# Kernel optimization log

Measured on AMD Instinct MI355X. Metric: run time of the kernel, lower is better.

Reference implementation:

```python
import jax, jax.numpy as jnp
import numpy as np

N = 50000   # nodes
E = 800000  # edges
F = 128     # feat_dim
I = 128     # internal_dim
G = 64      # graphs in batch
EPS = 1e-5


def setup_inputs() -> dict:
    key = jax.random.key(0)
    ks = jax.random.split(key, 32)
    s = 0.1
    inp = {
        'x': jax.random.normal(ks[0], (N, F), dtype=jnp.float32),
        'edge_index': jax.random.randint(ks[1], (2, E), 0, N, dtype=jnp.int64),
        'batch': jnp.sort(jax.random.randint(ks[2], (N,), 0, G, dtype=jnp.int64)),
        # InitialSubnet: Linear(F->I) + BN(I)
        'init_W': jax.random.normal(ks[3], (F, I)) * s,
        'init_b': jnp.zeros((I,)),
        'init_g': jnp.ones((I,)),
        'init_bt': jnp.zeros((I,)),
        # 2 middle EdgeConv subnets: Linear(2I->I) + BN(I)
        'mid_W': jax.random.normal(ks[4], (2, 2 * I, I)) * s,
        'mid_b': jnp.zeros((2, I)),
        'mid_g': jnp.ones((2, I)),
        'mid_bt': jnp.zeros((2, I)),
        # 1 er / 1 pr receptor-specific EdgeConv subnet each
        'er_W': jax.random.normal(ks[5], (1, 2 * I, I)) * s,
        'er_b': jnp.zeros((1, I)),
        'er_g': jnp.ones((1, I)),
        'er_bt': jnp.zeros((1, I)),
        'pr_W': jax.random.normal(ks[6], (1, 2 * I, I)) * s,
        'pr_b': jnp.zeros((1, I)),
        'pr_g': jnp.ones((1, I)),
        'pr_bt': jnp.zeros((1, I)),
        # 3 shared posts: Linear(I->2) + BN(2)
        'spost_W': jax.random.normal(ks[7], (3, I, 2)) * s,
        'spost_b': jnp.zeros((3, 2)),
        'spost_g': jnp.ones((3, 2)),
        'spost_bt': jnp.zeros((3, 2)),
        # 1 er post / 1 pr post: Linear(I->1) + BN(1)
        'erpost_W': jax.random.normal(ks[8], (1, I, 1)) * s,
        'erpost_b': jnp.zeros((1, 1)),
        'erpost_g': jnp.ones((1, 1)),
        'erpost_bt': jnp.zeros((1, 1)),
        'prpost_W': jax.random.normal(ks[9], (1, I, 1)) * s,
        'prpost_b': jnp.zeros((1, 1)),
        'prpost_g': jnp.ones((1, 1)),
        'prpost_bt': jnp.zeros((1, 1)),
    }
    return inp


def _bn(h, g, b):
    # BatchNorm1d in training mode: batch stats over the row dim, biased var
    m = jnp.mean(h, axis=0)
    v = jnp.var(h, axis=0)
    return (h - m) * jax.lax.rsqrt(v + EPS) * g + b


def _edgeconv(h, src, dst, W, b, g, bt):
    # PyG EdgeConv: msg = nn(cat([x_i, x_j - x_i])), aggr=max over incoming edges
    x_i = h[dst]                      # [E, I]
    x_j = h[src]                      # [E, I]
    msg = jnp.concatenate([x_i, x_j - x_i], axis=-1) @ W + b  # [E, I]
    msg = jax.nn.elu(_bn(msg, g, bt))
    out = jax.ops.segment_max(msg, dst, num_segments=N)
    return jnp.where(jnp.isneginf(out), 0.0, out)  # isolated nodes -> 0


def _post(h, batch, counts, W, b, g, bt):
    # elu(BN(Linear(h))) then global_mean_pool; dropout is identity (eval)
    h2 = jax.nn.elu(_bn(h @ W + b, g, bt))
    pooled = jax.ops.segment_sum(h2, batch, num_segments=G)
    return pooled / counts[:, None]


def reference(x, edge_index, batch,
              init_W, init_b, init_g, init_bt,
              mid_W, mid_b, mid_g, mid_bt,
              er_W, er_b, er_g, er_bt,
              pr_W, pr_b, pr_g, pr_bt,
              spost_W, spost_b, spost_g, spost_bt,
              erpost_W, erpost_b, erpost_g, erpost_bt,
              prpost_W, prpost_b, prpost_g, prpost_bt):
    src, dst = edge_index[0], edge_index[1]
    counts = jnp.maximum(jax.ops.segment_sum(jnp.ones((N,), x.dtype), batch, num_segments=G), 1.0)

    outs = []
    # InitialSubnet: gelu(BN(Linear(x)))
    h = jax.nn.gelu(_bn(x @ init_W + init_b, init_g, init_bt), approximate=False)
    outs.append(_post(h, batch, counts, spost_W[0], spost_b[0], spost_g[0], spost_bt[0]))

    for l in range(2):
        h = _edgeconv(h, src, dst, mid_W[l], mid_b[l], mid_g[l], mid_bt[l])
        outs.append(_post(h, batch, counts, spost_W[l + 1], spost_b[l + 1], spost_g[l + 1], spost_bt[l + 1]))

    er_h = h
    pr_h = h
    for l in range(1):
        er_h = _edgeconv(er_h, src, dst, er_W[l], er_b[l], er_g[l], er_bt[l])
        er_out = _post(er_h, batch, counts, erpost_W[l], erpost_b[l], erpost_g[l], erpost_bt[l])
        pr_h = _edgeconv(pr_h, src, dst, pr_W[l], pr_b[l], pr_g[l], pr_bt[l])
        pr_out = _post(pr_h, batch, counts, prpost_W[l], prpost_b[l], prpost_g[l], prpost_bt[l])
        outs.append(jnp.concatenate([er_out, pr_out], axis=-1))

    agg = outs[0]
    for o in outs[1:]:
        agg = agg + o
    return agg  # [G, 2]
```

## Files before the change

### kernel.cpp

```cpp
#include <hip/hip_runtime.h>
#include <math.h>

#define EPS 1e-5f

typedef float f32x4v __attribute__((ext_vector_type(4)));
typedef short s16x8  __attribute__((ext_vector_type(8)));

__device__ __forceinline__ float elu_f(float x) { return x > 0.f ? x : expm1f(x); }
__device__ __forceinline__ float blo(unsigned u) { return __uint_as_float(u << 16); }
__device__ __forceinline__ float bhi(unsigned u) { return __uint_as_float(u & 0xffff0000u); }
__device__ __forceinline__ unsigned f2b(float f) {
  unsigned u = __float_as_uint(f);
  unsigned r = ((u >> 16) & 1u) + 0x7fffu;
  return (u + r) >> 16;
}
__device__ __forceinline__ unsigned pack2(float a, float b) {
  return f2b(a) | (f2b(b) << 16);
}

__global__ __launch_bounds__(256) void prep_csr0(const float* __restrict__ init_W,
    const float* __restrict__ mid_W, const float* __restrict__ er_W,
    const float* __restrict__ pr_W, const float* __restrict__ mid_g,
    const float* __restrict__ er_g, const float* __restrict__ pr_g,
    unsigned short* __restrict__ WT,
// ... 12 lines not shown
    if (grp == 1)      { W = mid_W;             g = mid_g;       Wd = WT + 1 * 16384; W2 = WT + 2 * 16384; }
    else if (grp == 2) { W = mid_W + 256 * 128; g = mid_g + 128; Wd = WT + 3 * 16384; W2 = WT + 4 * 16384; }
    else if (grp == 3) { W = er_W;              g = er_g;        Wd = WT + 5 * 16384; W2 = WT + 6 * 16384; }
    else               { W = pr_W;              g = pr_g;        Wd = WT + 7 * 16384; W2 = WT + 8 * 16384; }
    float sg = (g[c] >= 0.f) ? 1.f : -1.f;
    float w1 = W[k * 128 + c];
    float w2 = W[(k + 128) * 128 + c];
    Wd[c * 128 + k] = (unsigned short)f2b((w1 - w2) * sg);
    W2[c * 128 + k] = (unsigned short)f2b(w2 * sg);
  } else {
    int b = blockIdx.x - 320;
    if (b < 64) {
      __shared__ int cnt[256];
      cnt[threadIdx.x] = 0;
      __syncthreads();
      int i0 = b * 256 + threadIdx.x, stride = 64 * 256;
      for (int e = i0; e < Ecnt; e += stride) atomicAdd(&cnt[(unsigned)dst[e] >> 8], 1);
      __syncthreads();
      partials[b * 256 + threadIdx.x] = cnt[threadIdx.x];
    } else {
      __shared__ float lc[64];
      if (threadIdx.x < 64) lc[threadIdx.x] = 0.f;
      __syncthreads();
      int i0 = (b - 64) * 256 + threadIdx.x, stride = 64 * 256;
      for (int n = i0; n < Nn; n += stride) atomicAdd(&lc[batch[n]], 1.f);
      __syncthreads();
      if (threadIdx.x < 64 && lc[threadIdx.x] != 0.f)
        atomicAdd(&counts[threadIdx.x * 16], lc[threadIdx.x]);
    }
  }
}

__global__ __launch_bounds__(256) void csr_p0_scan(const int* __restrict__ partials,
    int nblk, int* __restrict__ bucket_base, int* __restrict__ gcursor) {
  __shared__ int sc[256];
  int b = threadIdx.x;
  int s = 0;
  for (int k = 0; k < nblk; ++k) s += partials[k * 256 + b];
  sc[b] = s;
  __syncthreads();
  for (int off = 1; off < 256; off <<= 1) {
    int t = (b >= off) ? sc[b - off] : 0;
    __syncthreads();
    sc[b] += t;
    __syncthreads();
  }
  int excl = sc[b] - s;
  bucket_base[b] = excl;
  gcursor[b * 16] = excl;
  if (b == 255) bucket_base[256] = sc[255];
}

#define P1_CHUNK 4096
__global__ __launch_bounds__(256) void csr_p1_bin(const int* __restrict__ src,
    const int* __restrict__ dst, int* __restrict__ gcursor,
    unsigned* __restrict__ binned, int Ecnt) {
  __shared__ unsigned stage[P1_CHUNK];
  __shared__ int cnt[256], lbase[256], gbase[256], lcur[256], sc[256];
  int tid = threadIdx.x;
  int e0 = blockIdx.x * P1_CHUNK;
  int ecnt = Ecnt - e0; if (ecnt > P1_CHUNK) ecnt = P1_CHUNK;
  cnt[tid] = 0;
  __syncthreads();
  for (int i = tid; i < ecnt; i += 256) atomicAdd(&cnt[(unsigned)dst[e0 + i] >> 8], 1);
  __syncthreads();
  sc[tid] = cnt[tid];
  __syncthreads();
  for (int off = 1; off < 256; off <<= 1) {
    int t = (tid >= off) ? sc[tid - off] : 0;
    __syncthreads();
    sc[tid] += t;
    __syncthreads();
  }
  lbase[tid] = sc[tid] - cnt[tid];
  lcur[tid] = lbase[tid];
  gbase[tid] = (cnt[tid] > 0) ? atomicAdd(&gcursor[tid * 16], cnt[tid]) : 0;
  __syncthreads();
  for (int i = tid; i < ecnt; i += 256) {
    int d = dst[e0 + i], s = src[e0 + i];
    int bk = (unsigned)d >> 8;
    int p = atomicAdd(&lcur[bk], 1);
    stage[p] = ((unsigned)bk << 24) | ((unsigned)(d & 255) << 16) | (unsigned)s;
  }
  __syncthreads();
  for (int i = tid; i < ecnt; i += 256) {
    unsigned v = stage[i];
    int bk = v >> 24;
    binned[gbase[bk] + (i - lbase[bk])] = v;
  }
}

#define P2_CAP 12288
__global__ __launch_bounds__(256) void csr_p2_sort(const unsigned* __restrict__ binned,
    const int* __restrict__ bucket_base, unsigned short* __restrict__ csr_src,
    int* __restrict__ deg, int* __restrict__ rowstart, int Nn) {
  __shared__ unsigned short stage[P2_CAP];
  __shared__ int cnt[256], lbase[256], lcur[256], sc[256];
  int b = blockIdx.x, tid = threadIdx.x;
  int base = bucket_base[b];
  int bcnt = bucket_base[b + 1] - base;
  if (bcnt > P2_CAP) bcnt = P2_CAP;
  cnt[tid] = 0;
  __syncthreads();
  for (int i = tid; i < bcnt; i += 256) atomicAdd(&cnt[(binned[base + i] >> 16) & 255], 1);
  __syncthreads();
  sc[tid] = cnt[tid];
  __syncthreads();
  for (int off = 1; off < 256; off <<= 1) {
    int t = (tid >= off) ? sc[tid - off] : 0;
    __syncthreads();
    sc[tid] += t;
    __syncthreads();
  }
  lbase[tid] = sc[tid] - cnt[tid];
  lcur[tid] = lbase[tid];
  int node = b * 256 + tid;
  if (node < Nn) { deg[node] = cnt[tid]; rowstart[node] = base + lbase[tid]; }
  __syncthreads();
  for (int i = tid; i < bcnt; i += 256) {
    unsigned v = binned[base + i];
    int j = (v >> 16) & 255;
    int p = atomicAdd(&lcur[j], 1);
    stage[p] = (unsigned short)(v & 0xffffu);
  }
  __syncthreads();
  for (int i = tid; i < bcnt; i += 256) csr_src[base + i] = stage[i];
}

template<int XF32, int NMAT, int STATS>
__global__ __launch_bounds__(256, 3) void gemm_mfma(const void* __restrict__ Xv,
    const unsigned short* __restrict__ W0t, const unsigned short* __restrict__ W1t,
    const unsigned short* __restrict__ W2t, const unsigned short* __restrict__ W3t,
    unsigned short* __restrict__ Y0, unsigned short* __restrict__ Y1,
    unsigned short* __restrict__ Y2, unsigned short* __restrict__ Y3,
    float* __restrict__ stOut, int Nrows) {
  int tid = threadIdx.x, lane = tid & 63, wv = tid >> 6;
  int r0 = blockIdx.x * 64;
  int rlo = lane & 15, kg = lane >> 4;
  s16x8 zf = {0, 0, 0, 0, 0, 0, 0, 0};
  s16x8 af[4][4];
#pragma unroll
  for (int rg = 0; rg < 4; ++rg) {
    int arow = r0 + rg * 16 + rlo;
    if (arow < Nrows) {
      if (XF32) {
        const float* xr = (const float*)Xv + (size_t)arow * 128 + kg * 8;
#pragma unroll
        for (int s2 = 0; s2 < 4; ++s2) {
          float4 a = *(const float4*)(xr + s2 * 32);
          float4 b = *(const float4*)(xr + s2 * 32 + 4);
          s16x8 t;
          t[0] = (short)f2b(a.x); t[1] = (short)f2b(a.y);
          t[2] = (short)f2b(a.z); t[3] = (short)f2b(a.w);
          t[4] = (short)f2b(b.x); t[5] = (short)f2b(b.y);
          t[6] = (short)f2b(b.z); t[7] = (short)f2b(b.w);
          af[rg][s2] = t;
        }
      } else {
        const unsigned short* xr = (const unsigned short*)Xv + (size_t)arow * 128 + kg * 8;
#pragma unroll
        for (int s2 = 0; s2 < 4; ++s2) af[rg][s2] = *(const s16x8*)(xr + s2 * 32);
      }
    } else {
#pragma unroll
      for (int s2 = 0; s2 < 4; ++s2) af[rg][s2] = zf;
    }
  }
  const unsigned short* Ws[4] = {W0t, W1t, W2t, W3t};
  unsigned short* Ys[4] = {Y0, Y1, Y2, Y3};
#pragma unroll
  for (int o = 0; o < NMAT; ++o) {
    const unsigned short* Wt = Ws[o];
    unsigned short* Y = Ys[o];
#pragma unroll
    for (int t = 0; t < 2; ++t) {
      int nt = wv * 2 + t;
      const unsigned short* wp = Wt + (size_t)(nt * 16 + rlo) * 128 + kg * 8;
      s16x8 wf[4];
#pragma unroll
      for (int s2 = 0; s2 < 4; ++s2) wf[s2] = *(const s16x8*)(wp + s2 * 32);
      f32x4v acc[4];
#pragma unroll
      for (int rg = 0; rg < 4; ++rg) acc[rg] = (f32x4v){0.f, 0.f, 0.f, 0.f};
#pragma unroll
      for (int s2 = 0; s2 < 4; ++s2)
#pragma unroll
        for (int rg = 0; rg < 4; ++rg)
          acc[rg] = __builtin_amdgcn_mfma_f32_16x16x32_bf16(wf[s2], af[rg][s2], acc[rg], 0, 0, 0);
      float ps0 = 0.f, ps1 = 0.f, ps2 = 0.f, ps3 = 0.f;
      float pq0 = 0.f, pq1 = 0.f, pq2 = 0.f, pq3 = 0.f;
#pragma unroll
      for (int rg = 0; rg < 4; ++rg) {
        int arow = r0 + rg * 16 + rlo;
        if (arow < Nrows) {
          uint2 ov;
          ov.x = pack2(acc[rg][0], acc[rg][1]);
          ov.y = pack2(acc[rg][2], acc[rg][3]);
          *(uint2*)(Y + (size_t)arow * 128 + nt * 16 + kg * 4) = ov;
          if (STATS) {
            float y0 = blo(ov.x), y1 = bhi(ov.x), y2 = blo(ov.y), y3 = bhi(ov.y);
            ps0 += y0; pq0 += y0 * y0;
            ps1 += y1; pq1 += y1 * y1;
            ps2 += y2; pq2 += y2 * y2;
            ps3 += y3; pq3 += y3 * y3;
          }
        }
      }
      if (STATS) {
#pragma unroll
        for (int off = 1; off < 16; off <<= 1) {
          ps0 += __shfl_xor(ps0, off); pq0 += __shfl_xor(pq0, off);
          ps1 += __shfl_xor(ps1, off); pq1 += __shfl_xor(pq1, off);
          ps2 += __shfl_xor(ps2, off); pq2 += __shfl_xor(pq2, off);
          ps3 += __shfl_xor(ps3, off); pq3 += __shfl_xor(pq3, off);
        }
        if (rlo == 0) {
          int col = nt * 16 + kg * 4;
          float* sb = stOut + (size_t)(blockIdx.x & 15) * 256;
          atomicAdd(&sb[2 * col + 0], ps0); atomicAdd(&sb[2 * col + 1], pq0);
          atomicAdd(&sb[2 * (col + 1)], ps1); atomicAdd(&sb[2 * (col + 1) + 1], pq1);
          atomicAdd(&sb[2 * (col + 2)], ps2); atomicAdd(&sb[2 * (col + 2) + 1], pq2);
          atomicAdd(&sb[2 * (col + 3)], ps3); atomicAdd(&sb[2 * (col + 3) + 1], pq3);
        }
      }
    }
  }
}

template<int NMAT, int ACT>
__global__ __launch_bounds__(256, 3) void gemm_act(const unsigned short* __restrict__ Xv,
    const unsigned short* __restrict__ W0t, const unsigned short* __restrict__ W1t,
    const unsigned short* __restrict__ W2t, const unsigned short* __restrict__ W3t,
    unsigned short* __restrict__ Y0, unsigned short* __restrict__ Y1,
    unsigned short* __restrict__ Y2, unsigned short* __restrict__ Y3,
    const float* __restrict__ stn, const float* __restrict__ g,
    const float* __restrict__ bt, const int* __restrict__ deg,
    const float* __restrict__ Wp, float* __restrict__ zP, float* __restrict__ stp,
    float invCnt, int Nrows) {
  __shared__ unsigned short hl[64][136];
  __shared__ float lsc[128], lsh[128], lw0[128], lw1[128];
  __shared__ float red[4][4];
  int tid = threadIdx.x, lane = tid & 63, wv = tid >> 6;
  int r0 = blockIdx.x * 64;
  int rlo = lane & 15, kg = lane >> 4;
  if (tid < 128) {
    float sm = 0.f, sq = 0.f;
#pragma unroll
    for (int k = 0; k < 16; ++k) {
      sm += stn[k * 256 + 2 * tid];
      sq += stn[k * 256 + 2 * tid + 1];
    }
    float mean = sm * invCnt;
    float var = sq * invCnt - mean * mean;
    float sc = g[tid] * rsqrtf(var + EPS);
    float sh = bt[tid] - mean * sc;
    if (ACT == 2 && g[tid] < 0.f) sc = -sc;
    lsc[tid] = sc; lsh[tid] = sh;
    lw0[tid] = Wp[tid * 2]; lw1[tid] = Wp[tid * 2 + 1];
  }
  __syncthreads();
  {
    int row = tid >> 2, q = tid & 3;
    int arow = r0 + row;
    bool rok = arow < Nrows;
    int lrow = rok ? arow : 0;
    float live = 1.f;
    if (ACT == 2) live = (rok && deg[arow] > 0) ? 1.f : 0.f;
    else live = rok ? 1.f : 0.f;
    const uint4* xr = (const uint4*)(Xv + (size_t)lrow * 128 + q * 32);
    float dd0 = 0.f, dd1 = 0.f;
#pragma unroll
    for (int b = 0; b < 4; ++b) {
      uint4 v = xr[b];
      unsigned w[4] = {v.x, v.y, v.z, v.w};
      int cb = q * 32 + b * 8;
#pragma unroll
      for (int u = 0; u < 4; ++u) {
        int c = cb + 2 * u;
        float t0 = blo(w[u]) * lsc[c] + lsh[c];
        float t1 = bhi(w[u]) * lsc[c + 1] + lsh[c + 1];
        float y0, y1;
        if (ACT == 1) {
          y0 = 0.5f * t0 * (1.f + erff(t0 * 0.70710678118f));
          y1 = 0.5f * t1 * (1.f + erff(t1 * 0.70710678118f));
        } else {
          y0 = elu_f(t0); y1 = elu_f(t1);
        }
        y0 *= live; y1 *= live;
        *(unsigned*)&hl[row][c] = pack2(y0, y1);
        dd0 += y0 * lw0[c] + y1 * lw0[c + 1];
        dd1 += y0 * lw1[c] + y1 * lw1[c + 1];
      }
    }
    dd0 += __shfl_xor(dd0, 1); dd0 += __shfl_xor(dd0, 2);
    dd1 += __shfl_xor(dd1, 1); dd1 += __shfl_xor(dd1, 2);
    if (q == 0 && rok) {
// ... 3 lines not shown
    float s0v = (q == 0 && rok) ? dd0 : 0.f;
    float s1v = (q == 0 && rok) ? dd1 : 0.f;
    float q0v = s0v * s0v, q1v = s1v * s1v;
#pragma unroll
    for (int off = 4; off < 64; off <<= 1) {
      s0v += __shfl_xor(s0v, off); s1v += __shfl_xor(s1v, off);
      q0v += __shfl_xor(q0v, off); q1v += __shfl_xor(q1v, off);
    }
    if (lane == 0) { red[wv][0] = s0v; red[wv][1] = s1v; red[wv][2] = q0v; red[wv][3] = q1v; }
  }
  __syncthreads();
  if (tid < 4) {
    float v = red[0][tid] + red[1][tid] + red[2][tid] + red[3][tid];
    atomicAdd(&stp[tid * 64], v);
  }
  s16x8 af[4][4];
#pragma unroll
  for (int rg = 0; rg < 4; ++rg)
#pragma unroll
    for (int s2 = 0; s2 < 4; ++s2)
      af[rg][s2] = *(const s16x8*)&hl[rg * 16 + rlo][kg * 8 + s2 * 32];
  const unsigned short* Ws[4] = {W0t, W1t, W2t, W3t};
  unsigned short* Ys[4] = {Y0, Y1, Y2, Y3};
#pragma unroll
  for (int o = 0; o < NMAT; ++o) {
    const unsigned short* Wt = Ws[o];
    unsigned short* Y = Ys[o];
#pragma unroll
    for (int t = 0; t < 2; ++t) {
      int nt = wv * 2 + t;
      const unsigned short* wp = Wt + (size_t)(nt * 16 + rlo) * 128 + kg * 8;
      s16x8 wf[4];
#pragma unroll
      for (int s2 = 0; s2 < 4; ++s2) wf[s2] = *(const s16x8*)(wp + s2 * 32);
      f32x4v acc[4];
#pragma unroll
      for (int rg = 0; rg < 4; ++rg) acc[rg] = (f32x4v){0.f, 0.f, 0.f, 0.f};
#pragma unroll
      for (int s2 = 0; s2 < 4; ++s2)
#pragma unroll
        for (int rg = 0; rg < 4; ++rg)
          acc[rg] = __builtin_amdgcn_mfma_f32_16x16x32_bf16(wf[s2], af[rg][s2], acc[rg], 0, 0, 0);
#pragma unroll
      for (int rg = 0; rg < 4; ++rg) {
        int arow = r0 + rg * 16 + rlo;
        if (arow < Nrows) {
          uint2 ov;
          ov.x = pack2(acc[rg][0], acc[rg][1]);
          ov.y = pack2(acc[rg][2], acc[rg][3]);
          *(uint2*)(Y + (size_t)arow * 128 + nt * 16 + kg * 4) = ov;
        }
      }
    }
  }
}

__global__ __launch_bounds__(256, 8) void conv_pass(const unsigned short* __restrict__ A,
    const unsigned short* __restrict__ B, const unsigned short* __restrict__ csr_src,
    const int* __restrict__ rowstart, const int* __restrict__ deg,
    const float* __restrict__ g, unsigned short* __restrict__ Mx,
    float* __restrict__ st, int Nn, int convBlks,
    const float* __restrict__ zPp, const int* __restrict__ batch,
    const float* __restrict__ counts, const float* __restrict__ stpp,
    const float* __restrict__ g2, const float* __restrict__ bt2,
    float* __restrict__ out, float invN) {
  __shared__ float s_sum[128], s_ssq[128];
  int tid = threadIdx.x;
  if ((int)blockIdx.x >= convBlks) {
    __shared__ float lacc[128];
    if (tid < 128) lacc[tid] = 0.f;
    __syncthreads();
    float m0 = stpp[0] * invN, v0 = stpp[128] * invN - m0 * m0;
    float scale0 = g2[0] * rsqrtf(v0 + EPS), shift0 = bt2[0] - m0 * scale0;
    float m1 = stpp[64] * invN, v1 = stpp[192] * invN - m1 * m1;
    float scale1 = g2[1] * rsqrtf(v1 + EPS), shift1 = bt2[1] - m1 * scale1;
    int i0 = (blockIdx.x - convBlks) * 256 + tid;
    int stride = 32 * 256;
    for (int n = i0; n < Nn; n += stride) {
      int gi = batch[n];
      atomicAdd(&lacc[gi * 2], elu_f(zPp[n * 2] * scale0 + shift0));
      atomicAdd(&lacc[gi * 2 + 1], elu_f(zPp[n * 2 + 1] * scale1 + shift1));
    }
    __syncthreads();
    if (tid < 128) {
      int gi = tid >> 1, p = tid & 1;
      float v = lacc[tid];
      if (v != 0.f) atomicAdd(&out[gi * 2 + p], v / fmaxf(counts[gi * 16], 1.f));
    }
    return;
  }
  if (tid < 128) { s_sum[tid] = 0.f; s_ssq[tid] = 0.f; }
  __syncthreads();
  int lane = tid & 63;
  int wave = __builtin_amdgcn_readfirstlane((blockIdx.x << 2) + (tid >> 6));
  int wstride = convBlks << 2;
  int c0 = lane * 2;
  float sg0 = (g[c0] >= 0.f) ? 1.f : -1.f;
  float sg1 = (g[c0 + 1] >= 0.f) ? 1.f : -1.f;
  const unsigned* A32 = (const unsigned*)A;
  const unsigned* B32 = (const unsigned*)B;
  unsigned* M32 = (unsigned*)Mx;
  float s0 = 0.f, ss0 = 0.f, s1 = 0.f, ss1 = 0.f;
  for (int n = wave; n < Nn; n += wstride) {
    int dg = deg[n];
    if (dg == 0) continue;
    int beg = rowstart[n];
    unsigned ua = A32[(size_t)n * 64 + lane];
    float a0 = blo(ua), a1 = bhi(ua);
    float mx0 = -INFINITY, mx1 = -INFINITY;
    int e = beg, eend = beg + dg;
    for (; e + 8 <= eend; e += 8) {
      int idx[8];
#pragma unroll
      for (int q = 0; q < 8; ++q) idx[q] = csr_src[e + q];
      unsigned uu[8];
#pragma unroll
      for (int q = 0; q < 8; ++q) uu[q] = B32[(size_t)idx[q] * 64 + lane];
#pragma unroll
      for (int q = 0; q < 8; ++q) {
        float m0 = a0 + blo(uu[q]), m1 = a1 + bhi(uu[q]);
        s0 += m0; ss0 += m0 * m0;
        s1 += m1; ss1 += m1 * m1;
        mx0 = fmaxf(mx0, m0);
        mx1 = fmaxf(mx1, m1);
      }
    }
    for (; e + 2 <= eend; e += 2) {
      int ia = csr_src[e], ib = csr_src[e + 1];
      unsigned u0 = B32[(size_t)ia * 64 + lane];
      unsigned u1 = B32[(size_t)ib * 64 + lane];
      float m00 = a0 + blo(u0), m01 = a1 + bhi(u0);
      float m10 = a0 + blo(u1), m11 = a1 + bhi(u1);
      s0 += m00 + m10; ss0 += m00 * m00 + m10 * m10;
      s1 += m01 + m11; ss1 += m01 * m01 + m11 * m11;
      mx0 = fmaxf(mx0, fmaxf(m00, m10));
      mx1 = fmaxf(mx1, fmaxf(m01, m11));
    }
    if (e < eend) {
      unsigned u0 = B32[(size_t)csr_src[e] * 64 + lane];
      float m00 = a0 + blo(u0), m01 = a1 + bhi(u0);
      s0 += m00; ss0 += m00 * m00;
      s1 += m01; ss1 += m01 * m01;
      mx0 = fmaxf(mx0, m00);
      mx1 = fmaxf(mx1, m01);
    }
    M32[(size_t)n * 64 + lane] = pack2(mx0, mx1);
  }
  atomicAdd(&s_sum[c0], s0 * sg0); atomicAdd(&s_ssq[c0], ss0);
  atomicAdd(&s_sum[c0 + 1], s1 * sg1); atomicAdd(&s_ssq[c0 + 1], ss1);
  __syncthreads();
  if (tid < 128) {
    float* sb = st + (size_t)(blockIdx.x & 15) * 256;
    atomicAdd(&sb[2 * tid], s_sum[tid]);
    atomicAdd(&sb[2 * tid + 1], s_ssq[tid]);
  }
}

__global__ __launch_bounds__(256, 8) void conv_pass_dual(
    const unsigned short* __restrict__ Aer, const unsigned short* __restrict__ Ber,
    const unsigned short* __restrict__ Apr, const unsigned short* __restrict__ Bpr,
    const unsigned short* __restrict__ csr_src,
    const int* __restrict__ rowstart, const int* __restrict__ deg,
    const float* __restrict__ g_er, const float* __restrict__ g_pr,
    unsigned short* __restrict__ Mer, unsigned short* __restrict__ Mpr,
    float* __restrict__ st_er, float* __restrict__ st_pr, int Nn, int convBlks,
    const float* __restrict__ zPp, const int* __restrict__ batch,
    const float* __restrict__ counts, const float* __restrict__ stpp,
    const float* __restrict__ g2, const float* __restrict__ bt2,
    float* __restrict__ out, float invN) {
  __shared__ float s_e[256], s_p[256];
  int tid = threadIdx.x;
  if ((int)blockIdx.x >= convBlks) {
    __shared__ float lacc[128];
    if (tid < 128) lacc[tid] = 0.f;
    __syncthreads();
    float m0 = stpp[0] * invN, v0 = stpp[128] * invN - m0 * m0;
    float scale0 = g2[0] * rsqrtf(v0 + EPS), shift0 = bt2[0] - m0 * scale0;
    float m1 = stpp[64] * invN, v1 = stpp[192] * invN - m1 * m1;
    float scale1 = g2[1] * rsqrtf(v1 + EPS), shift1 = bt2[1] - m1 * scale1;
    int i0 = (blockIdx.x - convBlks) * 256 + tid;
    int stride = 32 * 256;
    for (int n = i0; n < Nn; n += stride) {
      int gi = batch[n];
      atomicAdd(&lacc[gi * 2], elu_f(zPp[n * 2] * scale0 + shift0));
      atomicAdd(&lacc[gi * 2 + 1], elu_f(zPp[n * 2 + 1] * scale1 + shift1));
    }
    __syncthreads();
    if (tid < 128) {
      int gi = tid >> 1, p = tid & 1;
      float v = lacc[tid];
      if (v != 0.f) atomicAdd(&out[gi * 2 + p], v / fmaxf(counts[gi * 16], 1.f));
    }
    return;
  }
  s_e[tid] = 0.f; s_p[tid] = 0.f;
  __syncthreads();
  int lane = tid & 63;
  int wave = __builtin_amdgcn_readfirstlane((blockIdx.x << 2) + (tid >> 6));
  int wstride = convBlks << 2;
  int c0 = lane * 2;
  float sge0 = (g_er[c0] >= 0.f) ? 1.f : -1.f;
  float sge1 = (g_er[c0 + 1] >= 0.f) ? 1.f : -1.f;
  float sgp0 = (g_pr[c0] >= 0.f) ? 1.f : -1.f;
  float sgp1 = (g_pr[c0 + 1] >= 0.f) ? 1.f : -1.f;
  const unsigned* Ae32 = (const unsigned*)Aer;
  const unsigned* Be32 = (const unsigned*)Ber;
  const unsigned* Ap32 = (const unsigned*)Apr;
  const unsigned* Bp32 = (const unsigned*)Bpr;
  unsigned* Me32 = (unsigned*)Mer;
  unsigned* Mp32 = (unsigned*)Mpr;
  float se0 = 0.f, sse0 = 0.f, se1 = 0.f, sse1 = 0.f;
  float sp0 = 0.f, ssp0 = 0.f, sp1 = 0.f, ssp1 = 0.f;
  for (int n = wave; n < Nn; n += wstride) {
    int dg = deg[n];
    if (dg == 0) continue;
    int beg = rowstart[n];
    unsigned uae = Ae32[(size_t)n * 64 + lane];
    unsigned uap = Ap32[(size_t)n * 64 + lane];
    float ae0 = blo(uae), ae1 = bhi(uae);
    float ap0 = blo(uap), ap1 = bhi(uap);
    float mxe0 = -INFINITY, mxe1 = -INFINITY, mxp0 = -INFINITY, mxp1 = -INFINITY;
    int e = beg, eend = beg + dg;
    for (; e + 8 <= eend; e += 8) {
      int idx[8];
#pragma unroll
      for (int q = 0; q < 8; ++q) idx[q] = csr_src[e + q];
      unsigned ue[8], up[8];
#pragma unroll
      for (int q = 0; q < 8; ++q) ue[q] = Be32[(size_t)idx[q] * 64 + lane];
#pragma unroll
      for (int q = 0; q < 8; ++q) up[q] = Bp32[(size_t)idx[q] * 64 + lane];
#pragma unroll
      for (int q = 0; q < 8; ++q) {
        float me0 = ae0 + blo(ue[q]), me1 = ae1 + bhi(ue[q]);
        float mp0 = ap0 + blo(up[q]), mp1 = ap1 + bhi(up[q]);
        se0 += me0; sse0 += me0 * me0; se1 += me1; sse1 += me1 * me1;
        sp0 += mp0; ssp0 += mp0 * mp0; sp1 += mp1; ssp1 += mp1 * mp1;
        mxe0 = fmaxf(mxe0, me0); mxe1 = fmaxf(mxe1, me1);
        mxp0 = fmaxf(mxp0, mp0); mxp1 = fmaxf(mxp1, mp1);
      }
    }
    for (; e + 2 <= eend; e += 2) {
      int i0 = csr_src[e], i1 = csr_src[e + 1];
      unsigned ue0 = Be32[(size_t)i0 * 64 + lane];
      unsigned up0 = Bp32[(size_t)i0 * 64 + lane];
      unsigned ue1 = Be32[(size_t)i1 * 64 + lane];
      unsigned up1 = Bp32[(size_t)i1 * 64 + lane];
      float me0 = ae0 + blo(ue0), me1 = ae1 + bhi(ue0);
      float mp0 = ap0 + blo(up0), mp1 = ap1 + bhi(up0);
      float ne0 = ae0 + blo(ue1), ne1 = ae1 + bhi(ue1);
      float np0 = ap0 + blo(up1), np1 = ap1 + bhi(up1);
      se0 += me0 + ne0; sse0 += me0 * me0 + ne0 * ne0;
      se1 += me1 + ne1; sse1 += me1 * me1 + ne1 * ne1;
      sp0 += mp0 + np0; ssp0 += mp0 * mp0 + np0 * np0;
      sp1 += mp1 + np1; ssp1 += mp1 * mp1 + np1 * np1;
      mxe0 = fmaxf(mxe0, fmaxf(me0, ne0)); mxe1 = fmaxf(mxe1, fmaxf(me1, ne1));
      mxp0 = fmaxf(mxp0, fmaxf(mp0, np0)); mxp1 = fmaxf(mxp1, fmaxf(mp1, np1));
    }
    if (e < eend) {
      int i0 = csr_src[e];
      unsigned ue = Be32[(size_t)i0 * 64 + lane];
      unsigned up = Bp32[(size_t)i0 * 64 + lane];
      float me0 = ae0 + blo(ue), me1 = ae1 + bhi(ue);
      float mp0 = ap0 + blo(up), mp1 = ap1 + bhi(up);
      se0 += me0; sse0 += me0 * me0; se1 += me1; sse1 += me1 * me1;
      sp0 += mp0; ssp0 += mp0 * mp0; sp1 += mp1; ssp1 += mp1 * mp1;
      mxe0 = fmaxf(mxe0, me0); mxe1 = fmaxf(mxe1, me1);
      mxp0 = fmaxf(mxp0, mp0); mxp1 = fmaxf(mxp1, mp1);
    }
    Me32[(size_t)n * 64 + lane] = pack2(mxe0, mxe1);
    Mp32[(size_t)n * 64 + lane] = pack2(mxp0, mxp1);
  }
  atomicAdd(&s_e[2 * c0], se0 * sge0);       atomicAdd(&s_e[2 * c0 + 1], sse0);
  atomicAdd(&s_e[2 * (c0 + 1)], se1 * sge1); atomicAdd(&s_e[2 * (c0 + 1) + 1], sse1);
  atomicAdd(&s_p[2 * c0], sp0 * sgp0);       atomicAdd(&s_p[2 * c0 + 1], ssp0);
  atomicAdd(&s_p[2 * (c0 + 1)], sp1 * sgp1); atomicAdd(&s_p[2 * (c0 + 1) + 1], ssp1);
  __syncthreads();
  {
    float* se = st_er + (size_t)(blockIdx.x & 15) * 256;
    float* sp = st_pr + (size_t)(blockIdx.x & 15) * 256;
    atomicAdd(&se[tid], s_e[tid]);
    atomicAdd(&sp[tid], s_p[tid]);
  }
}

__global__ __launch_bounds__(256) void fused_post16_dual(
    const unsigned short* __restrict__ Mer, const unsigned short* __restrict__ Mpr,
    const int* __restrict__ deg,
    const float* __restrict__ st_er, const float* __restrict__ st_pr,
    const float* __restrict__ g_er, const float* __restrict__ bt_er,
    const float* __restrict__ g_pr, const float* __restrict__ bt_pr,
    const float* __restrict__ Wer, const float* __restrict__ Wpr,
    float* __restrict__ zP, float* __restrict__ stp_er, float* __restrict__ stp_pr,
    int Nn, float invE) {
  __shared__ float sce_l[128], she_l[128], scp_l[128], shp_l[128];
  __shared__ float red[4][4];
  int tid = threadIdx.x;
  if (tid < 128) {
    float sme = 0.f, sqe = 0.f, smp = 0.f, sqp = 0.f;
#pragma unroll
    for (int k = 0; k < 16; ++k) {
      sme += st_er[k * 256 + 2 * tid];
      sqe += st_er[k * 256 + 2 * tid + 1];
      smp += st_pr[k * 256 + 2 * tid];
      sqp += st_pr[k * 256 + 2 * tid + 1];
    }
    float mean = sme * invE;
    float var = sqe * invE - mean * mean;
    float sc = g_er[tid] * rsqrtf(var + EPS);
    she_l[tid] = bt_er[tid] - mean * sc;
    sce_l[tid] = (g_er[tid] < 0.f) ? -sc : sc;
    mean = smp * invE;
    var = sqp * invE - mean * mean;
    sc = g_pr[tid] * rsqrtf(var + EPS);
    shp_l[tid] = bt_pr[tid] - mean * sc;
    scp_l[tid] = (g_pr[tid] < 0.f) ? -sc : sc;
  }
  __syncthreads();
  int sub = tid & 15, c0 = sub * 8;
  float sce[8], she[8], scp[8], shp[8], we[8], wp[8];
#pragma unroll
  for (int j = 0; j < 8; ++j) {
    sce[j] = sce_l[c0 + j]; she[j] = she_l[c0 + j];
    scp[j] = scp_l[c0 + j]; shp[j] = shp_l[c0 + j];
    we[j] = Wer[c0 + j]; wp[j] = Wpr[c0 + j];
  }
  int g0 = (blockIdx.x * 256 + tid) >> 4;
  int gstride = gridDim.x * 16;
  bool leader = (sub == 0);
// ... 63 lines not shown
  int stride = gridDim.x * 256;
  for (int n = i0; n < Nrows; n += stride) {
    int gi = batch[n];
    float y0 = elu_f(zP[n * 2] * scale0 + shift0);
    float y1 = elu_f(zP[n * 2 + 1] * scale1 + shift1);
    atomicAdd(&lacc[gi * 2], y0);
    atomicAdd(&lacc[gi * 2 + 1], y1);
  }
  __syncthreads();
  if (threadIdx.x < 128) {
    int gi = threadIdx.x >> 1, p = threadIdx.x & 1;
    float v = lacc[threadIdx.x];
    if (v != 0.f)
      atomicAdd(&out[gi * 2 + p], v / fmaxf(counts[gi * 16], 1.f));
  }
}

extern "C" void kernel_launch(void* const* d_in, const int* in_sizes, int n_in,
                              void* d_out, int out_size, void* d_ws, size_t ws_size,
                              hipStream_t stream) {
  const float* x       = (const float*)d_in[0];
  const int*   ei      = (const int*)d_in[1];
  const int*   batch   = (const int*)d_in[2];
  const float* init_W  = (const float*)d_in[3];
  const float* init_g  = (const float*)d_in[5];
  const float* init_bt = (const float*)d_in[6];
  const float* mid_W   = (const float*)d_in[7];
  const float* mid_g   = (const float*)d_in[9];
  const float* mid_bt  = (const float*)d_in[10];
  const float* er_W    = (const float*)d_in[11];
  const float* er_g    = (const float*)d_in[13];
  const float* er_bt   = (const float*)d_in[14];
  const float* pr_W    = (const float*)d_in[15];
  const float* pr_g    = (const float*)d_in[17];
  const float* pr_bt   = (const float*)d_in[18];
  const float* spost_W  = (const float*)d_in[19];
  const float* spost_g  = (const float*)d_in[21];
  const float* spost_bt = (const float*)d_in[22];
  const float* erpost_W  = (const float*)d_in[23];
  const float* erpost_g  = (const float*)d_in[25];
  const float* erpost_bt = (const float*)d_in[26];
  const float* prpost_W  = (const float*)d_in[27];
  const float* prpost_g  = (const float*)d_in[29];
  const float* prpost_bt = (const float*)d_in[30];

  int N = in_sizes[0] / 128;
  int E = in_sizes[1] / 2;
  float invN = 1.f / (float)N;
  float invE = 1.f / (float)E;
  float* out = (float*)d_out;

  const int CONV_BLKS = 2048;
  int nbuck = (N + 255) >> 8;

  size_t NB = (size_t)N * 128;
  unsigned short* TbI = (unsigned short*)d_ws;
  unsigned short* Tb0 = TbI + NB;
  unsigned short* Tb1 = Tb0 + NB;
  unsigned short* Tb2 = Tb1 + NB;
  unsigned short* Tb3 = Tb2 + NB;
  unsigned short* MxB = Tb3 + NB;
  unsigned short* MxB2 = MxB + NB;
  float* zP     = (float*)(MxB2 + NB);
  float* counts = zP + (size_t)2 * N;
  float* stats  = counts + 1024;
  float* post   = stats + 5 * 4096;
  unsigned short* WT = (unsigned short*)(post + 5 * 512);
  int* deg        = (int*)(WT + 9 * 16384);
  int* rowstart   = deg + N;
  int* bucketbase = rowstart + N;
  int* gcursor    = bucketbase + 320;
  int* partials   = gcursor + 256 * 16;
  unsigned* binned = (unsigned*)(partials + 64 * 256);
  unsigned short* csr_src = (unsigned short*)(binned + E);

  int gemmGrid = (N + 63) / 64;

  hipMemsetAsync(d_out, 0, out_size * sizeof(float), stream);
  hipMemsetAsync(counts, 0, (1024 + 5 * 4096 + 5 * 512) * sizeof(float), stream);

  const int* e_src = ei;
  const int* e_dst = ei + E;
  prep_csr0<<<448, 256, 0, stream>>>(init_W, mid_W, er_W, pr_W, mid_g, er_g, pr_g, WT,
                                     e_dst, partials, E, batch, counts, N);
  csr_p0_scan<<<1, 256, 0, stream>>>(partials, 64, bucketbase, gcursor);
  csr_p1_bin<<<(E + P1_CHUNK - 1) / P1_CHUNK, 256, 0, stream>>>(e_src, e_dst, gcursor, binned, E);
  csr_p2_sort<<<nbuck, 256, 0, stream>>>(binned, bucketbase, csr_src, deg, rowstart, N);

  gemm_mfma<1, 1, 1><<<gemmGrid, 256, 0, stream>>>((const void*)x, WT, nullptr, nullptr, nullptr,
                                                   TbI, nullptr, nullptr, nullptr, stats, N);

  gemm_act<2, 1><<<gemmGrid, 256, 0, stream>>>(TbI,
      WT + 1 * 16384, WT + 2 * 16384, nullptr, nullptr, Tb0, Tb1, nullptr, nullptr,
      stats, init_g, init_bt, deg, spost_W, zP, post + 0 * 512, invN, N);

  conv_pass<<<CONV_BLKS + 32, 256, 0, stream>>>(Tb0, Tb1, csr_src, rowstart, deg, mid_g,
      MxB, stats + 1 * 4096, N, CONV_BLKS,
      zP, batch, counts, post + 0 * 512, spost_g, spost_bt, out, invN);

  gemm_act<2, 2><<<gemmGrid, 256, 0, stream>>>(MxB,
      WT + 3 * 16384, WT + 4 * 16384, nullptr, nullptr, Tb0, Tb1, nullptr, nullptr,
      stats + 1 * 4096, mid_g, mid_bt, deg, spost_W + 256, zP, post + 1 * 512, invE, N);

  conv_pass<<<CONV_BLKS + 32, 256, 0, stream>>>(Tb0, Tb1, csr_src, rowstart, deg, mid_g + 128,
      MxB, stats + 2 * 4096, N, CONV_BLKS,
      zP, batch, counts, post + 1 * 512, spost_g + 2, spost_bt + 2, out, invN);

  gemm_act<4, 2><<<gemmGrid, 256, 0, stream>>>(MxB,
      WT + 5 * 16384, WT + 6 * 16384, WT + 7 * 16384, WT + 8 * 16384,
      Tb0, Tb1, Tb2, Tb3,
      stats + 2 * 4096, mid_g + 128, mid_bt + 128, deg, spost_W + 512,
      zP, post + 2 * 512, invE, N);

  conv_pass_dual<<<CONV_BLKS + 32, 256, 0, stream>>>(Tb0, Tb1, Tb2, Tb3, csr_src, rowstart, deg,
      er_g, pr_g, MxB, MxB2, stats + 3 * 4096, stats + 4 * 4096, N, CONV_BLKS,
      zP, batch, counts, post + 2 * 512, spost_g + 4, spost_bt + 4, out, invN);

  fused_post16_dual<<<512, 256, 0, stream>>>(MxB, MxB2, deg,
      stats + 3 * 4096, stats + 4 * 4096, er_g, er_bt, pr_g, pr_bt,
      erpost_W, prpost_W, zP, post + 3 * 512, post + 4 * 512, N, invE);
  post_phase2_dual<<<32, 256, 0, stream>>>(zP, batch, counts,
      post + 3 * 512, post + 4 * 512, erpost_g, erpost_bt, prpost_g, prpost_bt,
      out, N, invN);
}
```

Measured before the change: 385.5 us.

## Merge CSR build passes with init GEMMs and factor edge BN statistics algebraically

```diff
diff --git a/kernel.cpp b/kernel.cpp
--- a/kernel.cpp
+++ b/kernel.cpp
@@ -88,13 +88,13 @@
 }
 
 #define P1_CHUNK 4096
-__global__ __launch_bounds__(256) void csr_p1_bin(const int* __restrict__ src,
+__device__ __forceinline__ void csr_p1_body(int bid, const int* __restrict__ src,
     const int* __restrict__ dst, int* __restrict__ gcursor,
     unsigned* __restrict__ binned, int Ecnt) {
   __shared__ unsigned stage[P1_CHUNK];
   __shared__ int cnt[256], lbase[256], gbase[256], lcur[256], sc[256];
   int tid = threadIdx.x;
-  int e0 = blockIdx.x * P1_CHUNK;
+  int e0 = bid * P1_CHUNK;
   int ecnt = Ecnt - e0; if (ecnt > P1_CHUNK) ecnt = P1_CHUNK;
   cnt[tid] = 0;
   __syncthreads();
@@ -127,12 +127,12 @@
 }
 
 #define P2_CAP 12288
-__global__ __launch_bounds__(256) void csr_p2_sort(const unsigned* __restrict__ binned,
+__device__ __forceinline__ void csr_p2_body(int bid, const unsigned* __restrict__ binned,
     const int* __restrict__ bucket_base, unsigned short* __restrict__ csr_src,
     int* __restrict__ deg, int* __restrict__ rowstart, int Nn) {
   __shared__ unsigned short stage[P2_CAP];
   __shared__ int cnt[256], lbase[256], lcur[256], sc[256];
-  int b = blockIdx.x, tid = threadIdx.x;
+  int b = bid, tid = threadIdx.x;
   int base = bucket_base[b];
   int bcnt = bucket_base[b + 1] - base;
   if (bcnt > P2_CAP) bcnt = P2_CAP;
@@ -164,14 +164,14 @@
 }
 
 template<int XF32, int NMAT, int STATS>
-__global__ __launch_bounds__(256, 3) void gemm_mfma(const void* __restrict__ Xv,
+__device__ __forceinline__ void gemm_mfma_body(int bid, const void* __restrict__ Xv,
     const unsigned short* __restrict__ W0t, const unsigned short* __restrict__ W1t,
     const unsigned short* __restrict__ W2t, const unsigned short* __restrict__ W3t,
     unsigned short* __restrict__ Y0, unsigned short* __restrict__ Y1,
     unsigned short* __restrict__ Y2, unsigned short* __restrict__ Y3,
     float* __restrict__ stOut, int Nrows) {
   int tid = threadIdx.x, lane = tid & 63, wv = tid >> 6;
-  int r0 = blockIdx.x * 64;
+  int r0 = bid * 64;
   int rlo = lane & 15, kg = lane >> 4;
   s16x8 zf = {0, 0, 0, 0, 0, 0, 0, 0};
   s16x8 af[4][4];
@@ -252,7 +252,7 @@
         }
         if (rlo == 0) {
           int col = nt * 16 + kg * 4;
-          float* sb = stOut + (size_t)(blockIdx.x & 15) * 256;
+          float* sb = stOut + (size_t)(bid & 15) * 256;
           atomicAdd(&sb[2 * col + 0], ps0); atomicAdd(&sb[2 * col + 1], pq0);
           atomicAdd(&sb[2 * (col + 1)], ps1); atomicAdd(&sb[2 * (col + 1) + 1], pq1);
           atomicAdd(&sb[2 * (col + 2)], ps2); atomicAdd(&sb[2 * (col + 2) + 1], pq2);
@@ -264,7 +264,7 @@
 }
 
 template<int NMAT, int ACT>
-__global__ __launch_bounds__(256, 3) void gemm_act(const unsigned short* __restrict__ Xv,
+__device__ __forceinline__ void gemm_act_body(int bid, const unsigned short* __restrict__ Xv,
     const unsigned short* __restrict__ W0t, const unsigned short* __restrict__ W1t,
     const unsigned short* __restrict__ W2t, const unsigned short* __restrict__ W3t,
     unsigned short* __restrict__ Y0, unsigned short* __restrict__ Y1,
@@ -277,7 +277,7 @@
   __shared__ float lsc[128], lsh[128], lw0[128], lw1[128];
   __shared__ float red[4][4];
   int tid = threadIdx.x, lane = tid & 63, wv = tid >> 6;
-  int r0 = blockIdx.x * 64;
+  int r0 = bid * 64;
   int rlo = lane & 15, kg = lane >> 4;
   if (tid < 128) {
     float sm = 0.f, sq = 0.f;
@@ -387,6 +387,52 @@
         }
       }
     }
+  }
+}
+
+template<int NMAT, int ACT>
+__global__ __launch_bounds__(256, 3) void gemm_act(const unsigned short* __restrict__ Xv,
+    const unsigned short* __restrict__ W0t, const unsigned short* __restrict__ W1t,
+    const unsigned short* __restrict__ W2t, const unsigned short* __restrict__ W3t,
+    unsigned short* __restrict__ Y0, unsigned short* __restrict__ Y1,
+    unsigned short* __restrict__ Y2, unsigned short* __restrict__ Y3,
+    const float* __restrict__ stn, const float* __restrict__ g,
+    const float* __restrict__ bt, const int* __restrict__ deg,
+    const float* __restrict__ Wp, float* __restrict__ zP, float* __restrict__ stp,
+    float invCnt, int Nrows) {
+  gemm_act_body<NMAT, ACT>(blockIdx.x, Xv, W0t, W1t, W2t, W3t, Y0, Y1, Y2, Y3,
+                           stn, g, bt, deg, Wp, zP, stp, invCnt, Nrows);
+}
+
+__global__ __launch_bounds__(256, 3) void p1_initgemm(
+    const int* __restrict__ src, const int* __restrict__ dst, int* __restrict__ gcursor,
+    unsigned* __restrict__ binned, int Ecnt, int p1b,
+    const void* __restrict__ Xv, const unsigned short* __restrict__ W0t,
+    unsigned short* __restrict__ Y0, float* __restrict__ stOut, int Nrows) {
+  if ((int)blockIdx.x < p1b) {
+    csr_p1_body(blockIdx.x, src, dst, gcursor, binned, Ecnt);
+  } else {
+    gemm_mfma_body<1, 1, 1>(blockIdx.x - p1b, Xv, W0t, nullptr, nullptr, nullptr,
+                            Y0, nullptr, nullptr, nullptr, stOut, Nrows);
+  }
+}
+
+__global__ __launch_bounds__(256, 3) void p2_act0(
+    const unsigned* __restrict__ binned, const int* __restrict__ bucket_base,
+    unsigned short* __restrict__ csr_src, int* __restrict__ deg,
+    int* __restrict__ rowstart, int Nn, int nbuck,
+    const unsigned short* __restrict__ Xv,
+    const unsigned short* __restrict__ W0t, const unsigned short* __restrict__ W1t,
+    unsigned short* __restrict__ Y0, unsigned short* __restrict__ Y1,
+    const float* __restrict__ stn, const float* __restrict__ g,
+    const float* __restrict__ bt, const float* __restrict__ Wp,
+    float* __restrict__ zP, float* __restrict__ stp, float invCnt) {
+  if ((int)blockIdx.x < nbuck) {
+    csr_p2_body(blockIdx.x, binned, bucket_base, csr_src, deg, rowstart, Nn);
+  } else {
+    gemm_act_body<2, 1>(blockIdx.x - nbuck, Xv, W0t, W1t, nullptr, nullptr,
+                        Y0, Y1, nullptr, nullptr, stn, g, bt, nullptr,
+                        Wp, zP, stp, invCnt, Nn);
   }
 }
 
@@ -435,13 +481,18 @@
   const unsigned* A32 = (const unsigned*)A;
   const unsigned* B32 = (const unsigned*)B;
   unsigned* M32 = (unsigned*)Mx;
-  float s0 = 0.f, ss0 = 0.f, s1 = 0.f, ss1 = 0.f;
+  float rP0 = 0.f, rP1 = 0.f;
+  float rQ0 = 0.f, rQ1 = 0.f;
+  float rC0 = 0.f, rC1 = 0.f;
+  float rT0 = 0.f, rT1 = 0.f;
+  float rB0 = 0.f, rB1 = 0.f;
   for (int n = wave; n < Nn; n += wstride) {
     int dg = deg[n];
     if (dg == 0) continue;
     int beg = rowstart[n];
     unsigned ua = A32[(size_t)n * 64 + lane];
     float a0 = blo(ua), a1 = bhi(ua);
+    float T0 = 0.f, T1 = 0.f;
     float mx0 = -INFINITY, mx1 = -INFINITY;
     int e = beg, eend = beg + dg;
     for (; e + 8 <= eend; e += 8) {
@@ -453,36 +504,41 @@
       for (int q = 0; q < 8; ++q) uu[q] = B32[(size_t)idx[q] * 64 + lane];
 #pragma unroll
       for (int q = 0; q < 8; ++q) {
-        float m0 = a0 + blo(uu[q]), m1 = a1 + bhi(uu[q]);
-        s0 += m0; ss0 += m0 * m0;
-        s1 += m1; ss1 += m1 * m1;
-        mx0 = fmaxf(mx0, m0);
-        mx1 = fmaxf(mx1, m1);
+        float b0 = blo(uu[q]), b1 = bhi(uu[q]);
+        T0 += b0; T1 += b1;
+        rB0 += b0 * b0; rB1 += b1 * b1;
+        mx0 = fmaxf(mx0, b0); mx1 = fmaxf(mx1, b1);
       }
     }
     for (; e + 2 <= eend; e += 2) {
       int ia = csr_src[e], ib = csr_src[e + 1];
       unsigned u0 = B32[(size_t)ia * 64 + lane];
       unsigned u1 = B32[(size_t)ib * 64 + lane];
-      float m00 = a0 + blo(u0), m01 = a1 + bhi(u0);
-      float m10 = a0 + blo(u1), m11 = a1 + bhi(u1);
-      s0 += m00 + m10; ss0 += m00 * m00 + m10 * m10;
-      s1 += m01 + m11; ss1 += m01 * m01 + m11 * m11;
-      mx0 = fmaxf(mx0, fmaxf(m00, m10));
-      mx1 = fmaxf(mx1, fmaxf(m01, m11));
+      float b00 = blo(u0), b01 = bhi(u0);
+      float b10 = blo(u1), b11 = bhi(u1);
+      T0 += b00 + b10; T1 += b01 + b11;
+      rB0 += b00 * b00 + b10 * b10; rB1 += b01 * b01 + b11 * b11;
+      mx0 = fmaxf(mx0, fmaxf(b00, b10));
+      mx1 = fmaxf(mx1, fmaxf(b01, b11));
     }
     if (e < eend) {
       unsigned u0 = B32[(size_t)csr_src[e] * 64 + lane];
-      float m00 = a0 + blo(u0), m01 = a1 + bhi(u0);
-      s0 += m00; ss0 += m00 * m00;
-      s1 += m01; ss1 += m01 * m01;
-      mx0 = fmaxf(mx0, m00);
-      mx1 = fmaxf(mx1, m01);
-    }
-    M32[(size_t)n * 64 + lane] = pack2(mx0, mx1);
-  }
-  atomicAdd(&s_sum[c0], s0 * sg0); atomicAdd(&s_ssq[c0], ss0);
-  atomicAdd(&s_sum[c0 + 1], s1 * sg1); atomicAdd(&s_ssq[c0 + 1], ss1);
+      float b00 = blo(u0), b01 = bhi(u0);
+      T0 += b00; T1 += b01;
+      rB0 += b00 * b00; rB1 += b01 * b01;
+      mx0 = fmaxf(mx0, b00); mx1 = fmaxf(mx1, b01);
+    }
+    float fdg = (float)dg;
+    rP0 += fdg * a0; rP1 += fdg * a1;
+    rQ0 += fdg * a0 * a0; rQ1 += fdg * a1 * a1;
+    rC0 += a0 * T0; rC1 += a1 * T1;
+    rT0 += T0; rT1 += T1;
+    M32[(size_t)n * 64 + lane] = pack2(a0 + mx0, a1 + mx1);
+  }
+  atomicAdd(&s_sum[c0], (rP0 + rT0) * sg0);
+  atomicAdd(&s_ssq[c0], rQ0 + 2.f * rC0 + rB0);
+  atomicAdd(&s_sum[c0 + 1], (rP1 + rT1) * sg1);
+  atomicAdd(&s_ssq[c0 + 1], rQ1 + 2.f * rC1 + rB1);
   __syncthreads();
   if (tid < 128) {
     float* sb = st + (size_t)(blockIdx.x & 15) * 256;
@@ -544,8 +600,11 @@
   const unsigned* Bp32 = (const unsigned*)Bpr;
   unsigned* Me32 = (unsigned*)Mer;
   unsigned* Mp32 = (unsigned*)Mpr;
-  float se0 = 0.f, sse0 = 0.f, se1 = 0.f, sse1 = 0.f;
-  float sp0 = 0.f, ssp0 = 0.f, sp1 = 0.f, ssp1 = 0.f;
+  float rPe0 = 0.f, rPe1 = 0.f, rPp0 = 0.f, rPp1 = 0.f;
+  float rQe0 = 0.f, rQe1 = 0.f, rQp0 = 0.f, rQp1 = 0.f;
+  float rCe0 = 0.f, rCe1 = 0.f, rCp0 = 0.f, rCp1 = 0.f;
+  float rTe0 = 0.f, rTe1 = 0.f, rTp0 = 0.f, rTp1 = 0.f;
+  float rBe0 = 0.f, rBe1 = 0.f, rBp0 = 0.f, rBp1 = 0.f;
   for (int n = wave; n < Nn; n += wstride) {
     int dg = deg[n];
     if (dg == 0) continue;
@@ -554,6 +613,7 @@
     unsigned uap = Ap32[(size_t)n * 64 + lane];
     float ae0 = blo(uae), ae1 = bhi(uae);
     float ap0 = blo(uap), ap1 = bhi(uap);
+    float Te0 = 0.f, Te1 = 0.f, Tp0 = 0.f, Tp1 = 0.f;
     float mxe0 = -INFINITY, mxe1 = -INFINITY, mxp0 = -INFINITY, mxp1 = -INFINITY;
     int e = beg, eend = beg + dg;
     for (; e + 8 <= eend; e += 8) {
@@ -567,12 +627,13 @@
       for (int q = 0; q < 8; ++q) up[q] = Bp32[(size_t)idx[q] * 64 + lane];
 #pragma unroll
       for (int q = 0; q < 8; ++q) {
-        float me0 = ae0 + blo(ue[q]), me1 = ae1 + bhi(ue[q]);
-        float mp0 = ap0 + blo(up[q]), mp1 = ap1 + bhi(up[q]);
-        se0 += me0; sse0 += me0 * me0; se1 += me1; sse1 += me1 * me1;
-        sp0 += mp0; ssp0 += mp0 * mp0; sp1 += mp1; ssp1 += mp1 * mp1;
-        mxe0 = fmaxf(mxe0, me0); mxe1 = fmaxf(mxe1, me1);
-        mxp0 = fmaxf(mxp0, mp0); mxp1 = fmaxf(mxp1, mp1);
+        float be0 = blo(ue[q]), be1 = bhi(ue[q]);
+        float bp0 = blo(up[q]), bp1 = bhi(up[q]);
+        Te0 += be0; Te1 += be1; Tp0 += bp0; Tp1 += bp1;
+        rBe0 += be0 * be0; rBe1 += be1 * be1;
+        rBp0 += bp0 * bp0; rBp1 += bp1 * bp1;
+        mxe0 = fmaxf(mxe0, be0); mxe1 = fmaxf(mxe1, be1);
+        mxp0 = fmaxf(mxp0, bp0); mxp1 = fmaxf(mxp1, bp1);
       }
     }
     for (; e + 2 <= eend; e += 2) {
@@ -581,35 +642,48 @@
       unsigned up0 = Bp32[(size_t)i0 * 64 + lane];
       unsigned ue1 = Be32[(size_t)i1 * 64 + lane];
       unsigned up1 = Bp32[(size_t)i1 * 64 + lane];
-      float me0 = ae0 + blo(ue0), me1 = ae1 + bhi(ue0);
-      float mp0 = ap0 + blo(up0), mp1 = ap1 + bhi(up0);
-      float ne0 = ae0 + blo(ue1), ne1 = ae1 + bhi(ue1);
-      float np0 = ap0 + blo(up1), np1 = ap1 + bhi(up1);
-      se0 += me0 + ne0; sse0 += me0 * me0 + ne0 * ne0;
-      se1 += me1 + ne1; sse1 += me1 * me1 + ne1 * ne1;
-      sp0 += mp0 + np0; ssp0 += mp0 * mp0 + np0 * np0;
-      sp1 += mp1 + np1; ssp1 += mp1 * mp1 + np1 * np1;
-      mxe0 = fmaxf(mxe0, fmaxf(me0, ne0)); mxe1 = fmaxf(mxe1, fmaxf(me1, ne1));
-      mxp0 = fmaxf(mxp0, fmaxf(mp0, np0)); mxp1 = fmaxf(mxp1, fmaxf(mp1, np1));
+      float be00 = blo(ue0), be01 = bhi(ue0);
+      float bp00 = blo(up0), bp01 = bhi(up0);
+      float be10 = blo(ue1), be11 = bhi(ue1);
+      float bp10 = blo(up1), bp11 = bhi(up1);
+      Te0 += be00 + be10; Te1 += be01 + be11;
+      Tp0 += bp00 + bp10; Tp1 += bp01 + bp11;
+      rBe0 += be00 * be00 + be10 * be10; rBe1 += be01 * be01 + be11 * be11;
+      rBp0 += bp00 * bp00 + bp10 * bp10; rBp1 += bp01 * bp01 + bp11 * bp11;
+      mxe0 = fmaxf(mxe0, fmaxf(be00, be10)); mxe1 = fmaxf(mxe1, fmaxf(be01, be11));
+      mxp0 = fmaxf(mxp0, fmaxf(bp00, bp10)); mxp1 = fmaxf(mxp1, fmaxf(bp01, bp11));
     }
     if (e < eend) {
       int i0 = csr_src[e];
-      unsigned ue = Be32[(size_t)i0 * 64 + lane];
-      unsigned up = Bp32[(size_t)i0 * 64 + lane];
-      float me0 = ae0 + blo(ue), me1 = ae1 + bhi(ue);
-      float mp0 = ap0 + blo(up), mp1 = ap1 + bhi(up);
-      se0 += me0; sse0 += me0 * me0; se1 += me1; sse1 += me1 * me1;
-      sp0 += mp0; ssp0 += mp0 * mp0; sp1 += mp1; ssp1 += mp1 * mp1;
-      mxe0 = fmaxf(mxe0, me0); mxe1 = fmaxf(mxe1, me1);
-      mxp0 = fmaxf(mxp0, mp0); mxp1 = fmaxf(mxp1, mp1);
-    }
-    Me32[(size_t)n * 64 + lane] = pack2(mxe0, mxe1);
-    Mp32[(size_t)n * 64 + lane] = pack2(mxp0, mxp1);
-  }
-  atomicAdd(&s_e[2 * c0], se0 * sge0);       atomicAdd(&s_e[2 * c0 + 1], sse0);
-  atomicAdd(&s_e[2 * (c0 + 1)], se1 * sge1); atomicAdd(&s_e[2 * (c0 + 1) + 1], sse1);
-  atomicAdd(&s_p[2 * c0], sp0 * sgp0);       atomicAdd(&s_p[2 * c0 + 1], ssp0);
-  atomicAdd(&s_p[2 * (c0 + 1)], sp1 * sgp1); atomicAdd(&s_p[2 * (c0 + 1) + 1], ssp1);
+      unsigned ue0 = Be32[(size_t)i0 * 64 + lane];
+      unsigned up0 = Bp32[(size_t)i0 * 64 + lane];
+      float be00 = blo(ue0), be01 = bhi(ue0);
+      float bp00 = blo(up0), bp01 = bhi(up0);
+      Te0 += be00; Te1 += be01; Tp0 += bp00; Tp1 += bp01;
+      rBe0 += be00 * be00; rBe1 += be01 * be01;
+      rBp0 += bp00 * bp00; rBp1 += bp01 * bp01;
+      mxe0 = fmaxf(mxe0, be00); mxe1 = fmaxf(mxe1, be01);
+      mxp0 = fmaxf(mxp0, bp00); mxp1 = fmaxf(mxp1, bp01);
+    }
+    float fdg = (float)dg;
+    rPe0 += fdg * ae0; rPe1 += fdg * ae1;
+    rPp0 += fdg * ap0; rPp1 += fdg * ap1;
+    rQe0 += fdg * ae0 * ae0; rQe1 += fdg * ae1 * ae1;
+    rQp0 += fdg * ap0 * ap0; rQp1 += fdg * ap1 * ap1;
+    rCe0 += ae0 * Te0; rCe1 += ae1 * Te1;
+    rCp0 += ap0 * Tp0; rCp1 += ap1 * Tp1;
+    rTe0 += Te0; rTe1 += Te1; rTp0 += Tp0; rTp1 += Tp1;
+    Me32[(size_t)n * 64 + lane] = pack2(ae0 + mxe0, ae1 + mxe1);
+    Mp32[(size_t)n * 64 + lane] = pack2(ap0 + mxp0, ap1 + mxp1);
+  }
+  atomicAdd(&s_e[2 * c0], (rPe0 + rTe0) * sge0);
+  atomicAdd(&s_e[2 * c0 + 1], rQe0 + 2.f * rCe0 + rBe0);
+  atomicAdd(&s_e[2 * (c0 + 1)], (rPe1 + rTe1) * sge1);
+  atomicAdd(&s_e[2 * (c0 + 1) + 1], rQe1 + 2.f * rCe1 + rBe1);
+  atomicAdd(&s_p[2 * c0], (rPp0 + rTp0) * sgp0);
+  atomicAdd(&s_p[2 * c0 + 1], rQp0 + 2.f * rCp0 + rBp0);
+  atomicAdd(&s_p[2 * (c0 + 1)], (rPp1 + rTp1) * sgp1);
+  atomicAdd(&s_p[2 * (c0 + 1) + 1], rQp1 + 2.f * rCp1 + rBp1);
   __syncthreads();
   {
     float* se = st_er + (size_t)(blockIdx.x & 15) * 256;
@@ -779,6 +853,7 @@
 
   const int CONV_BLKS = 2048;
   int nbuck = (N + 255) >> 8;
+  int p1b = (E + P1_CHUNK - 1) / P1_CHUNK;
 
   size_t NB = (size_t)N * 128;
   unsigned short* TbI = (unsigned short*)d_ws;
@@ -811,15 +886,13 @@
   prep_csr0<<<448, 256, 0, stream>>>(init_W, mid_W, er_W, pr_W, mid_g, er_g, pr_g, WT,
                                      e_dst, partials, E, batch, counts, N);
   csr_p0_scan<<<1, 256, 0, stream>>>(partials, 64, bucketbase, gcursor);
-  csr_p1_bin<<<(E + P1_CHUNK - 1) / P1_CHUNK, 256, 0, stream>>>(e_src, e_dst, gcursor, binned, E);
-  csr_p2_sort<<<nbuck, 256, 0, stream>>>(binned, bucketbase, csr_src, deg, rowstart, N);
-
-  gemm_mfma<1, 1, 1><<<gemmGrid, 256, 0, stream>>>((const void*)x, WT, nullptr, nullptr, nullptr,
-                                                   TbI, nullptr, nullptr, nullptr, stats, N);
-
-  gemm_act<2, 1><<<gemmGrid, 256, 0, stream>>>(TbI,
-      WT + 1 * 16384, WT + 2 * 16384, nullptr, nullptr, Tb0, Tb1, nullptr, nullptr,
-      stats, init_g, init_bt, deg, spost_W, zP, post + 0 * 512, invN, N);
+
+  p1_initgemm<<<p1b + gemmGrid, 256, 0, stream>>>(e_src, e_dst, gcursor, binned, E, p1b,
+      (const void*)x, WT, TbI, stats, N);
+
+  p2_act0<<<nbuck + gemmGrid, 256, 0, stream>>>(binned, bucketbase, csr_src, deg, rowstart,
+      N, nbuck, TbI, WT + 1 * 16384, WT + 2 * 16384, Tb0, Tb1,
+      stats, init_g, init_bt, spost_W, zP, post + 0 * 512, invN);
 
   conv_pass<<<CONV_BLKS + 32, 256, 0, stream>>>(Tb0, Tb1, csr_src, rowstart, deg, mid_g,
       MxB, stats + 1 * 4096, N, CONV_BLKS,
```

Measured after the change: 403.0 us. 1.05x slower.
